# Kernel optimization log

Measured on AMD Instinct MI355X. Metric: run time of the kernel, lower is better.

Reference implementation:

```python
import jax, jax.numpy as jnp
import numpy as np

H = 1024          # hidden_size
NH = 16           # num_attention_heads
HD = H // NH      # head_dim = 64
CAUSAL_HEADS = 4  # causal_attention_heads
META_HEADS = NH // 4
B, S = 2, 2048
CVEC = 16
# static cognitive-state scalars (Python floats in the original dict)
CAUSAL_WEIGHT = 0.7   # > 0.5 -> causal branch active
AWARENESS = 0.9       # > 0.8 -> metacognitive branch active


def _mha(x, in_w, in_b, out_w, out_b, n_heads):
    """torch nn.MultiheadAttention (batch_first, self-attn, no mask, eval).
    in_w: [H, 3H] (pre-transposed), out_w: [H, H]."""
    b, s, h = x.shape
    hd = h // n_heads
    qkv = x @ in_w + in_b                      # [b, s, 3H]
    q, k, v = jnp.split(qkv, 3, axis=-1)
    def heads(t):
        return t.reshape(b, s, n_heads, hd).transpose(0, 2, 1, 3)  # [b, nh, s, hd]
    q, k, v = heads(q), heads(k), heads(v)
    scores = jnp.einsum('bhqd,bhkd->bhqk', q, k) / jnp.sqrt(jnp.float32(hd))
    probs = jax.nn.softmax(scores, axis=-1)
    ctx = jnp.einsum('bhqk,bhkd->bhqd', probs, v)
    ctx = ctx.transpose(0, 2, 1, 3).reshape(b, s, h)
    return ctx @ out_w + out_b


def setup_inputs() -> dict:
    key = jax.random.key(0)
    ks = jax.random.split(key, 20)
    w = lambda k, shp: (jax.random.normal(k, shp, dtype=jnp.float32) * 0.02)
    inp = {
        'hidden_states': jax.random.normal(ks[0], (B, S, H), dtype=jnp.float32),
        'attention_mask': jnp.ones((B, S), dtype=jnp.int32),
        'consciousness_vector': jax.random.uniform(ks[1], (CVEC,), dtype=jnp.float32),
        'Wq': w(ks[2], (H, H)), 'bq': jnp.zeros((H,), jnp.float32),
        'Wk': w(ks[3], (H, H)), 'bk': jnp.zeros((H,), jnp.float32),
        'Wv': w(ks[4], (H, H)), 'bv': jnp.zeros((H,), jnp.float32),
        'Wg': w(ks[5], (H, NH)), 'bg': jnp.zeros((NH,), jnp.float32),
        'Wa': w(ks[6], (CVEC, NH)), 'ba': jnp.zeros((NH,), jnp.float32),
        'ca_in_w': w(ks[7], (H, 3 * H)), 'ca_in_b': jnp.zeros((3 * H,), jnp.float32),
        'ca_out_w': w(ks[8], (H, H)), 'ca_out_b': jnp.zeros((H,), jnp.float32),
        'ma_in_w': w(ks[9], (H, 3 * H)), 'ma_in_b': jnp.zeros((3 * H,), jnp.float32),
        'ma_out_w': w(ks[10], (H, H)), 'ma_out_b': jnp.zeros((H,), jnp.float32),
        'Wo': w(ks[11], (H, H)), 'bo': jnp.zeros((H,), jnp.float32),
    }
    return inp


def reference(hidden_states, attention_mask, consciousness_vector,
              Wq, bq, Wk, bk, Wv, bv, Wg, bg, Wa, ba,
              ca_in_w, ca_in_b, ca_out_w, ca_out_b,
              ma_in_w, ma_in_b, ma_out_w, ma_out_b, Wo, bo):
    b, s, h = hidden_states.shape
    def heads(t):
        return t.reshape(b, s, NH, HD).transpose(0, 2, 1, 3)  # [b, NH, s, HD]
    q = heads(hidden_states @ Wq + bq)
    k = heads(hidden_states @ Wk + bk)
    v = heads(hidden_states @ Wv + bv)
    scores = jnp.einsum('bhqd,bhkd->bhqk', q, k) / jnp.sqrt(jnp.float32(HD))
    # consciousness modulation: sigmoid(gate(hs) + awareness(cvec)) -> [b, s, NH]
    gate = hidden_states @ Wg + bg
    awareness = consciousness_vector @ Wa + ba            # [NH]
    modulation = jax.nn.sigmoid(gate + awareness)         # [b, s, NH]
    # per-head, per-query-row scaling of scores ([b, NH, s, 1])
    scores = scores * modulation.transpose(0, 2, 1)[:, :, :, None]
    # mask: [b, s] -> [b, 1, 1, s]; masked positions -> -inf before softmax
    scores = jnp.where(attention_mask[:, None, None, :] == 0, -jnp.inf, scores)
    probs = jax.nn.softmax(scores, axis=-1)
    # dropout is identity in eval mode
    ctx = jnp.einsum('bhqk,bhkd->bhqd', probs, v)
    ctx = ctx.transpose(0, 2, 1, 3).reshape(b, s, h)
    # causal branch (causal_active > 0.5)
    causal_ctx = _mha(hidden_states, ca_in_w, ca_in_b, ca_out_w, ca_out_b, CAUSAL_HEADS)
    ctx = ctx * (1.0 - CAUSAL_WEIGHT) + causal_ctx * CAUSAL_WEIGHT
    # metacognitive branch (awareness_level > 0.8)
    meta_ctx = _mha(ctx, ma_in_w, ma_in_b, ma_out_w, ma_out_b, META_HEADS)
    mw = (AWARENESS - 0.8) / 0.2
    ctx = ctx * (1.0 - mw * 0.3) + meta_ctx * (mw * 0.3)
    return ctx @ Wo + bo
```

## Files before the change

kernel.cpp:

```cpp
#include <hip/hip_runtime.h>
#include <math.h>

#define HDIM 1024
#define NHEAD 16
#define SEQ   2048
#define BATCH 2
#define NROWS (BATCH * SEQ)
#define NEG_INF (-__builtin_inff())

typedef unsigned short u16;
typedef float  f32x4  __attribute__((ext_vector_type(4)));
typedef short  short8 __attribute__((ext_vector_type(8)));
typedef _Float16 half8 __attribute__((ext_vector_type(8)));

__device__ __forceinline__ u16 f2bf(float x) {
    unsigned u = __float_as_uint(x);
    unsigned r = u + 0x7fffu + ((u >> 16) & 1u);
    return (u16)(r >> 16);
}
__device__ __forceinline__ float bf2f(u16 h) { return __uint_as_float(((unsigned)h) << 16); }
__device__ __forceinline__ u16 f2h(float x) { _Float16 h = (_Float16)x; return *(u16*)&h; }

__global__ __launch_bounds__(256) void conv_f16(const float* __restrict__ src,
                                                u16* __restrict__ dst)
{
    int i8 = (blockIdx.x * 256 + threadIdx.x) * 8;
    float4 a = *(const float4*)&src[i8];
    float4 b = *(const float4*)&src[i8 + 4];
    u16 h[8] = {f2h(a.x), f2h(a.y), f2h(a.z), f2h(a.w),
                f2h(b.x), f2h(b.y), f2h(b.z), f2h(b.w)};
    uint4 p;
    p.x = h[0] | (h[1] << 16); p.y = h[2] | (h[3] << 16);
    p.z = h[4] | (h[5] << 16); p.w = h[6] | (h[7] << 16);
    *(uint4*)&dst[i8] = p;
}

__global__ __launch_bounds__(256) void convW(const float* __restrict__ Wsrc, int ldw, int n0,
                                             int dst, u16* __restrict__ WTH, u16* __restrict__ WTL)
{
    __shared__ float tile[64][65];
    int t = threadIdx.x;
    int nb = blockIdx.x * 64, kb = blockIdx.y * 64;
    #pragma unroll
    for (int i = 0; i < 4; i++) {
        int r = (t >> 4) + i * 16, cg = t & 15;
        float4 v = *(const float4*)&Wsrc[(size_t)(kb + r) * ldw + n0 + nb + cg * 4];
        tile[r][cg * 4 + 0] = v.x; tile[r][cg * 4 + 1] = v.y;
        tile[r][cg * 4 + 2] = v.z; tile[r][cg * 4 + 3] = v.w;
    }
    __syncthreads();
    int n = t & 63, g0 = (t >> 6) * 2;
    #pragma unroll
    for (int gg = 0; gg < 2; gg++) {
        int g = g0 + gg;
        u16 hi[8], lo[8];
        #pragma unroll
        for (int u = 0; u < 8; u++) {
            float x = tile[g * 8 + u][n];
            hi[u] = f2bf(x); lo[u] = f2bf(x - bf2f(hi[u]));
        }
        size_t ob = (size_t)(dst + nb + n) * 1024 + kb + g * 8;
        uint4 ph, pl;
        ph.x = hi[0] | (hi[1] << 16); ph.y = hi[2] | (hi[3] << 16);
        ph.z = hi[4] | (hi[5] << 16); ph.w = hi[6] | (hi[7] << 16);
        pl.x = lo[0] | (lo[1] << 16); pl.y = lo[2] | (lo[3] << 16);
        pl.z = lo[4] | (lo[5] << 16); pl.w = lo[6] | (lo[7] << 16);
        *(uint4*)&WTH[ob] = ph;
        *(uint4*)&WTL[ob] = pl;
    }
}

__global__ __launch_bounds__(256) void convW3_f16(
    const float* __restrict__ w0, const float* __restrict__ w1, const float* __restrict__ w2,
    int ldw, int n0s, u16* __restrict__ WT)
{
    __shared__ float tile[64][65];
    int t = threadIdx.x;
    int z = blockIdx.z;
    const float* Wsrc = (z == 0) ? w0 : (z == 1) ? w1 : w2;
    int n0 = z * n0s, dst = z * 1024;
    int nb = blockIdx.x * 64, kb = blockIdx.y * 64;
    #pragma unroll
    for (int i = 0; i < 4; i++) {
        int r = (t >> 4) + i * 16, cg = t & 15;
        float4 v = *(const float4*)&Wsrc[(size_t)(kb + r) * ldw + n0 + nb + cg * 4];
        tile[r][cg * 4 + 0] = v.x; tile[r][cg * 4 + 1] = v.y;
        tile[r][cg * 4 + 2] = v.z; tile[r][cg * 4 + 3] = v.w;
    }
    __syncthreads();
    int n = t & 63, g0 = (t >> 6) * 2;
    #pragma unroll
    for (int gg = 0; gg < 2; gg++) {
        int g = g0 + gg;
        u16 h[8];
        #pragma unroll
        for (int u = 0; u < 8; u++) h[u] = f2h(tile[g * 8 + u][n]);
        size_t ob = (size_t)(dst + nb + n) * 1024 + kb + g * 8;
        uint4 p;
        p.x = h[0] | (h[1] << 16); p.y = h[2] | (h[3] << 16);
        p.z = h[4] | (h[5] << 16); p.w = h[6] | (h[7] << 16);
        *(uint4*)&WT[ob] = p;
    }
}

__global__ __launch_bounds__(256) void transpose_f16(
    const u16* __restrict__ in, u16* __restrict__ out)
{
    __shared__ u16 th[64][72];
    int t = threadIdx.x;
    int cb = blockIdx.x * 64;
    int rb = blockIdx.y * 64;
    {
        int r = t >> 2;
        #pragma unroll
        for (int i = 0; i < 2; i++) {
            int ck = (t & 3) + 4 * i;
            *(short8*)&th[r][ck * 8] = *(const short8*)&in[(size_t)(rb + r) * 3072 + 2048 + cb + ck * 8];
        }
    }
    __syncthreads();
    int c = t & 63, g0 = (t >> 6) * 2;
    #pragma unroll
    for (int gg = 0; gg < 2; gg++) {
        int g = g0 + gg;
        u16 hv[8];
        #pragma unroll
        for (int u = 0; u < 8; u++) hv[u] = th[g * 8 + u][c];
        size_t ob = (size_t)(cb + c) * NROWS + rb + g * 8;
        uint4 ph;
        ph.x = hv[0] | (hv[1] << 16); ph.y = hv[2] | (hv[3] << 16);
        ph.z = hv[4] | (hv[5] << 16); ph.w = hv[6] | (hv[7] << 16);
        *(uint4*)&out[ob] = ph;
    }
}

__global__ __launch_bounds__(256) void gate_f32(
    const float* __restrict__ hs, const float* __restrict__ Wg,
    const float* __restrict__ bg, const float* __restrict__ cvec,
    const float* __restrict__ Wa, const float* __restrict__ ba,
    float* __restrict__ mod)
{
    __shared__ float aw[16];
    int t = threadIdx.x;
    if (t < 16) {
        float s = ba[t];
        for (int i = 0; i < 16; i++) s = fmaf(cvec[i], Wa[i * 16 + t], s);
        aw[t] = s;
    }
    __syncthreads();
    int h = t & 15;
    int r = blockIdx.x * 16 + (t >> 4);
    const float* hrow = hs + (size_t)r * HDIM;
    float s = bg[h];
    for (int k = 0; k < HDIM; k++) s = fmaf(hrow[k], Wg[k * 16 + h], s);
    s += aw[h];
    mod[(size_t)r * 16 + h] = 1.f / (1.f + __expf(-s));
}

__global__ __launch_bounds__(256, 3) void gemm_f16(
    const u16* __restrict__ A, const u16* __restrict__ BT,
    const float* __restrict__ b0, const float* __restrict__ b1, const float* __restrict__ b2,
    u16* __restrict__ out, int M, int N, int K)
{
    __shared__ u16 aS[128][40], bS[128][40];
    int t = threadIdx.x;
    int l = t & 63, w = t >> 6;
    int lane15 = l & 15, quad = l >> 4;
    int wm = (w >> 1) * 64, wn = (w & 1) * 64;
    int m0 = blockIdx.y * 128, n0 = blockIdx.x * 128;
    int sr = t >> 1;
    f32x4 acc[4][4] = {};
    short8 pa[2], pb[2];
    auto pre = [&](int k0) {
        #pragma unroll
        for (int i = 0; i < 2; i++) {
            int ck = (t & 1) * 2 + i;
            pa[i] = *(const short8*)&A[(size_t)(m0 + sr) * K + k0 + ck * 8];
            pb[i] = *(const short8*)&BT[(size_t)(n0 + sr) * K + k0 + ck * 8];
        }
    };
    pre(0);
    for (int k0 = 0; k0 < K; k0 += 32) {
        __syncthreads();
        #pragma unroll
        for (int i = 0; i < 2; i++) {
            int ck = (t & 1) * 2 + i;
            *(short8*)&aS[sr][ck * 8] = pa[i];
            *(short8*)&bS[sr][ck * 8] = pb[i];
        }
        __syncthreads();
        if (k0 + 32 < K) pre(k0 + 32);
        half8 af[4], bf[4];
        #pragma unroll
        for (int mt = 0; mt < 4; mt++)
            af[mt] = *(const half8*)&aS[wm + mt * 16 + lane15][quad * 8];
        #pragma unroll
        for (int nt = 0; nt < 4; nt++)
            bf[nt] = *(const half8*)&bS[wn + nt * 16 + lane15][quad * 8];
        #pragma unroll
        for (int mt = 0; mt < 4; mt++)
            #pragma unroll
            for (int nt = 0; nt < 4; nt++)
                acc[mt][nt] = __builtin_amdgcn_mfma_f32_16x16x32_f16(af[mt], bf[nt], acc[mt][nt], 0, 0, 0);
    }
    #pragma unroll
    for (int nt = 0; nt < 4; nt++) {
        int col = n0 + wn + nt * 16 + lane15;
        const float* bsel = (col < 1024) ? b0 : (col < 2048) ? b1 : b2;
        float bv = bsel[col & 1023];
        #pragma unroll
        for (int mt = 0; mt < 4; mt++)
            #pragma unroll
            for (int reg = 0; reg < 4; reg++) {
                int row = m0 + wm + mt * 16 + quad * 4 + reg;
                out[(size_t)row * N + col] = f2h(acc[mt][nt][reg] + bv);
            }
    }
}

__global__ __launch_bounds__(256, 2) void gemm_bf3(
    const u16* __restrict__ AH, const u16* __restrict__ AL,
    const u16* __restrict__ BTH, const u16* __restrict__ BTL,
    const float* __restrict__ bias,
    const u16* __restrict__ CinH, const u16* __restrict__ CinL,
    float* __restrict__ outF, u16* __restrict__ outH, u16* __restrict__ outL,
    u16* __restrict__ outX,
    int M, int N, int K, float alpha, float beta, int omode)
{
    __shared__ u16 aH[128][40], aL[128][40], bH[128][40], bL[128][40];
    int t = threadIdx.x;
    int l = t & 63, w = t >> 6;
    int lane15 = l & 15, quad = l >> 4;
    int wm = (w >> 1) * 64, wn = (w & 1) * 64;
    int m0 = blockIdx.y * 128, n0 = blockIdx.x * 128;
    int sr = t >> 1;
    f32x4 acc[4][4] = {};
    short8 pah[2], pal[2], pbh[2], pbl[2];

    auto pre = [&](int k0) {
        #pragma unroll
        for (int i = 0; i < 2; i++) {
            int ck = (t & 1) * 2 + i;
            size_t ga = (size_t)(m0 + sr) * K + k0 + ck * 8;
            size_t gb = (size_t)(n0 + sr) * K + k0 + ck * 8;
            pah[i] = *(const short8*)&AH[ga];
            pal[i] = *(const short8*)&AL[ga];
            pbh[i] = *(const short8*)&BTH[gb];
            pbl[i] = *(const short8*)&BTL[gb];
        }
    };
    pre(0);
    for (int k0 = 0; k0 < K; k0 += 32) {
        __syncthreads();
        #pragma unroll
        for (int i = 0; i < 2; i++) {
            int ck = (t & 1) * 2 + i;
            *(short8*)&aH[sr][ck * 8] = pah[i];
            *(short8*)&aL[sr][ck * 8] = pal[i];
            *(short8*)&bH[sr][ck * 8] = pbh[i];
            *(short8*)&bL[sr][ck * 8] = pbl[i];
        }
        __syncthreads();
        if (k0 + 32 < K) pre(k0 + 32);
        short8 afh[4], afl[4], bfh[4], bfl[4];
        #pragma unroll
        for (int mt = 0; mt < 4; mt++) {
            int r = wm + mt * 16 + lane15;
            afh[mt] = *(const short8*)&aH[r][quad * 8];
            afl[mt] = *(const short8*)&aL[r][quad * 8];
        }
        #pragma unroll
        for (int nt = 0; nt < 4; nt++) {
            int r = wn + nt * 16 + lane15;
            bfh[nt] = *(const short8*)&bH[r][quad * 8];
            bfl[nt] = *(const short8*)&bL[r][quad * 8];
        }
        #pragma unroll
        for (int mt = 0; mt < 4; mt++)
            #pragma unroll
            for (int nt = 0; nt < 4; nt++) {
                acc[mt][nt] = __builtin_amdgcn_mfma_f32_16x16x32_bf16(afh[mt], bfh[nt], acc[mt][nt], 0, 0, 0);
                acc[mt][nt] = __builtin_amdgcn_mfma_f32_16x16x32_bf16(afh[mt], bfl[nt], acc[mt][nt], 0, 0, 0);
                acc[mt][nt] = __builtin_amdgcn_mfma_f32_16x16x32_bf16(afl[mt], bfh[nt], acc[mt][nt], 0, 0, 0);
            }
    }
    #pragma unroll
    for (int nt = 0; nt < 4; nt++) {
        int col = n0 + wn + nt * 16 + lane15;
        float bv = bias[col];
        #pragma unroll
        for (int mt = 0; mt < 4; mt++) {
            #pragma unroll
            for (int reg = 0; reg < 4; reg++) {
                int row = m0 + wm + mt * 16 + quad * 4 + reg;
                size_t idx = (size_t)row * N + col;
                float v = alpha * (acc[mt][nt][reg] + bv);
                if (beta != 0.f) v += beta * (bf2f(CinH[idx]) + bf2f(CinL[idx]));
                if (omode == 0) outF[idx] = v;
                else {
                    u16 hb = f2bf(v);
                    outH[idx] = hb;
                    outL[idx] = f2bf(v - bf2f(hb));
                }
                if (outX) outX[idx] = f2h(v);
            }
        }
    }
}

__global__ __launch_bounds__(256, 3) void attn_main(
    const u16* __restrict__ QKV, const u16* __restrict__ VT,
    const float* __restrict__ modp, const int* __restrict__ maskp, float scale,
    u16* __restrict__ outH, u16* __restrict__ outL)
{
    constexpr int NT = SEQ / 128;
    constexpr int LD = 3 * HDIM;
    __shared__ __align__(16) u16 kbuf[2][128][64];
    __shared__ u16 st[4][16][132];

    int t = threadIdx.x, l = t & 63, w = t >> 6;
    int lane15 = l & 15, quad = l >> 4;
    int qt0 = blockIdx.x * 64, h = blockIdx.y, b = blockIdx.z;
    int bS_ = b * SEQ;
    int srK = t >> 1, ckK = (t & 1) * 4;
    int srV = t >> 2, ckV = (t & 3) * 4;

    half8 qf[2];
    {
        size_t qoff = (size_t)(bS_ + qt0 + w * 16 + lane15) * LD + h * 64 + quad * 8;
        qf[0] = *(const half8*)&QKV[qoff];
        qf[1] = *(const half8*)&QKV[qoff + 32];
    }
    float smod2[4];
    #pragma unroll
    for (int reg = 0; reg < 4; reg++) {
        int rw = qt0 + w * 16 + quad * 4 + reg;
        smod2[reg] = scale * 1.44269504f * modp[(size_t)(bS_ + rw) * NHEAD + h];
    }
    float lst[4] = {0.f, 0.f, 0.f, 0.f};
    f32x4 o[4] = {};

    short8 ph[4];
    auto loadK = [&](int kt) {
        size_t base = (size_t)(bS_ + kt + srK) * LD + HDIM + h * 64;
        #pragma unroll
        for (int i = 0; i < 4; i++) ph[i] = *(const short8*)&QKV[base + (ckK + i) * 8];
    };
    auto loadV = [&](int kt) {
        size_t base = (size_t)(h * 64 + srV) * NROWS + bS_ + kt;
        #pragma unroll
        for (int i = 0; i < 4; i++) ph[i] = *(const short8*)&VT[base + (ckV + i) * 8];
    };
    auto storK = [&](int pb) {
        #pragma unroll
        for (int i = 0; i < 4; i++) {
            int cw = (ckK + i) ^ (srK & 7);
            *(short8*)&kbuf[pb][srK][cw * 8] = ph[i];
        }
    };
    auto storV = [&](int pb) {
        u16* vb = &kbuf[pb][0][0];
        #pragma unroll
        for (int i = 0; i < 4; i++) {
            int cw = (ckV + i) ^ (srV & 7);
            *(short8*)&vb[srV * 128 + cw * 8] = ph[i];
        }
    };

    loadK(0); storK(0); loadV(0);
    int pb = 0;

    for (int it = 0; it < NT; it++) {
        int kt = it * 128;
        __syncthreads();
        storV(pb ^ 1);
        if (it + 1 < NT) loadK(kt + 128);
        f32x4 sacc[8] = {};
        #pragma unroll
        for (int ks = 0; ks < 2; ks++)
            #pragma unroll
            for (int nb = 0; nb < 8; nb++) {
                int r = nb * 16 + lane15;
                int cw = (ks * 4 + quad) ^ (r & 7);
                half8 kb = *(const half8*)&kbuf[pb][r][cw * 8];
                sacc[nb] = __builtin_amdgcn_mfma_f32_16x16x32_f16(qf[ks], kb, sacc[nb], 0, 0, 0);
            }
        pb ^= 1;
        #pragma unroll
        for (int nb = 0; nb < 8; nb++) {
            float kmf = maskp[bS_ + kt + nb * 16 + lane15] ? 1.f : 0.f;
            #pragma unroll
            for (int reg = 0; reg < 4; reg++) {
                float p = exp2f(fmaf(sacc[nb][reg], smod2[reg], -6.f)) * kmf;
                st[w][quad * 4 + reg][nb * 16 + lane15] = f2h(p);
                lst[reg] += p;
            }
        }
        half8 pf[4];
        #pragma unroll
        for (int ks = 0; ks < 4; ks++)
            pf[ks] = *(const half8*)&st[w][lane15][ks * 32 + quad * 8];
        __syncthreads();
        if (it + 1 < NT) { storK(pb ^ 1); loadV(kt + 128); }
        const u16* vb = &kbuf[pb][0][0];
        #pragma unroll
        for (int ks = 0; ks < 4; ks++)
            #pragma unroll
            for (int nb = 0; nb < 4; nb++) {
                int r = nb * 16 + lane15;
                int cw = (ks * 4 + quad) ^ (r & 7);
                half8 vv = *(const half8*)&vb[r * 128 + cw * 8];
                o[nb] = __builtin_amdgcn_mfma_f32_16x16x32_f16(pf[ks], vv, o[nb], 0, 0, 0);
            }
        pb ^= 1;
    }
    #pragma unroll
    for (int d = 1; d < 16; d <<= 1)
        #pragma unroll
        for (int reg = 0; reg < 4; reg++)
            lst[reg] += __shfl_xor(lst[reg], d, 64);
    #pragma unroll
    for (int reg = 0; reg < 4; reg++) {
        float inv = (lst[reg] > 0.f) ? 1.f / lst[reg] : 0.f;
        int row = qt0 + w * 16 + quad * 4 + reg;
        size_t rbase = (size_t)(bS_ + row) * HDIM + h * 64;
        #pragma unroll
        for (int nb = 0; nb < 4; nb++) {
            float v = o[nb][reg] * inv;
            size_t idx = rbase + nb * 16 + lane15;
            u16 hb = f2bf(v);
            outH[idx] = hb;
            outL[idx] = f2bf(v - bf2f(hb));
        }
    }
}

template <int NC>
__global__ __launch_bounds__(256, 2) void attn_f16(
    const u16* __restrict__ QKV, const u16* __restrict__ VT,
    float scale, u16* __restrict__ outH, u16* __restrict__ outL, int ldo)
{
    constexpr int HDT = NC * 64;
    constexpr int NT  = (SEQ / 2) / 64;
    constexpr int LD  = 3 * HDIM;
    __shared__ __align__(16) u16 kbuf[2][2][64][64];
    __shared__ u16 st[4][16][68];
    __shared__ float xl[2][16];

    int t = threadIdx.x, l = t & 63, w = t >> 6;
    int lane15 = l & 15, quad = l >> 4;
    int g = w & 1, s = w >> 1;
    int t128 = t & 127, srow = t128 >> 1, ckb = (t128 & 1) * 4;
    int qt0 = blockIdx.x * 32, h = blockIdx.y, b = blockIdx.z;
    int bS = b * SEQ, kbeg = s * (SEQ / 2);

    half8 qf[NC][2];
    {
        size_t qoff = (size_t)(bS + qt0 + g * 16 + lane15) * LD + h * HDT + quad * 8;
        #pragma unroll
        for (int c = 0; c < NC; c++)
            #pragma unroll
            for (int ks = 0; ks < 2; ks++)
                qf[c][ks] = *(const half8*)&QKV[qoff + c * 64 + ks * 32];
    }
    float sc2 = scale * 1.44269504f;
    float lst[4] = {0.f, 0.f, 0.f, 0.f};
    f32x4 o[NC][4] = {};

    short8 phv[4];
    auto loadK = [&](int c, int kt) {
        size_t base = (size_t)(bS + kt + srow) * LD + HDIM + h * HDT + c * 64;
        #pragma unroll
        for (int i = 0; i < 4; i++) phv[i] = *(const short8*)&QKV[base + (ckb + i) * 8];
    };
    auto loadV = [&](int c, int kt) {
        size_t base = (size_t)(h * HDT + c * 64 + srow) * NROWS + bS + kt;
        #pragma unroll
        for (int i = 0; i < 4; i++) phv[i] = *(const short8*)&VT[base + (ckb + i) * 8];
    };
    auto stor = [&](int pb_) {
        #pragma unroll
        for (int i = 0; i < 4; i++) {
            int ck = ckb + i, cw = ck ^ (srow & 7);
            *(short8*)&kbuf[pb_][s][srow][cw * 8] = phv[i];
        }
    };

    loadK(0, kbeg);
    stor(0);
    loadK(1, kbeg);
    int pb = 0;

    for (int it = 0; it < NT; it++) {
        int kt = kbeg + it * 64;
        f32x4 sacc[4] = {};
        #pragma unroll
        for (int c = 0; c < NC; c++) {
            __syncthreads();
            stor(pb ^ 1);
            if (c + 2 < NC) loadK(c + 2, kt);
            else if (c + 2 < 2 * NC) loadV(c + 2 - NC, kt);
            else if (it + 1 < NT) loadK(0, kt + 64);
            #pragma unroll
            for (int ks = 0; ks < 2; ks++)
                #pragma unroll
                for (int nb = 0; nb < 4; nb++) {
                    int r = nb * 16 + lane15;
                    int cw = (ks * 4 + quad) ^ (r & 7);
                    half8 kb = *(const half8*)&kbuf[pb][s][r][cw * 8];
                    sacc[nb] = __builtin_amdgcn_mfma_f32_16x16x32_f16(qf[c][ks], kb, sacc[nb], 0, 0, 0);
                }
            pb ^= 1;
        }
        #pragma unroll
        for (int nb = 0; nb < 4; nb++)
            #pragma unroll
            for (int reg = 0; reg < 4; reg++) {
                float p = exp2f(fmaf(sacc[nb][reg], sc2, -6.f));
                st[w][quad * 4 + reg][nb * 16 + lane15] = f2h(p);
                lst[reg] += p;
            }
        half8 pf[2];
        #pragma unroll
        for (int ks = 0; ks < 2; ks++)
            pf[ks] = *(const half8*)&st[w][lane15][ks * 32 + quad * 8];
        #pragma unroll
        for (int c = 0; c < NC; c++) {
            __syncthreads();
            if (it < NT - 1 || c < NC - 1) stor(pb ^ 1);
            if (c + 2 < NC) loadV(c + 2, kt);
            else if (it + 1 < NT) {
                int p2 = c + 2 - NC;
                if (p2 < NC) loadK(p2, kt + 64); else loadV(p2 - NC, kt + 64);
            }
            #pragma unroll
            for (int ks = 0; ks < 2; ks++)
                #pragma unroll
                for (int nb = 0; nb < 4; nb++) {
                    int r = nb * 16 + lane15;
                    int cw = (ks * 4 + quad) ^ (r & 7);
                    half8 vb = *(const half8*)&kbuf[pb][s][r][cw * 8];
                    o[c][nb] = __builtin_amdgcn_mfma_f32_16x16x32_f16(pf[ks], vb, o[c][nb], 0, 0, 0);
                }
            pb ^= 1;
        }
    }
    #pragma unroll
    for (int d = 1; d < 16; d <<= 1)
        #pragma unroll
        for (int reg = 0; reg < 4; reg++)
            lst[reg] += __shfl_xor(lst[reg], d, 64);
    float* xO = (float*)kbuf;
    __syncthreads();
    if (s == 1) {
        #pragma unroll
        for (int c = 0; c < NC; c++)
            #pragma unroll
            for (int nb = 0; nb < 4; nb++)
                #pragma unroll
                for (int reg = 0; reg < 4; reg++)
                    xO[(size_t)(g * 16 + quad * 4 + reg) * HDT + c * 64 + nb * 16 + lane15] = o[c][nb][reg];
        if (lane15 == 0)
            #pragma unroll
            for (int reg = 0; reg < 4; reg++)
                xl[g][quad * 4 + reg] = lst[reg];
    }
    __syncthreads();
    if (s == 0) {
        #pragma unroll
        for (int reg = 0; reg < 4; reg++) {
            float lt = lst[reg] + xl[g][quad * 4 + reg];
            float inv = (lt > 0.f) ? 1.f / lt : 0.f;
            int row = qt0 + g * 16 + quad * 4 + reg;
            size_t rbase = (size_t)(bS + row) * ldo + h * HDT;
            #pragma unroll
            for (int c = 0; c < NC; c++)
                #pragma unroll
                for (int nb = 0; nb < 4; nb++) {
                    float x1 = xO[(size_t)(g * 16 + quad * 4 + reg) * HDT + c * 64 + nb * 16 + lane15];
                    float v = (o[c][nb][reg] + x1) * inv;
                    size_t idx = rbase + c * 64 + nb * 16 + lane15;
                    u16 hb = f2bf(v);
                    outH[idx] = hb;
                    outL[idx] = f2bf(v - bf2f(hb));
                }
        }
    }
}

extern "C" void kernel_launch(void* const* d_in, const int* in_sizes, int n_in,
                              void* d_out, int out_size, void* d_ws, size_t ws_size,
                              hipStream_t stream)
{
    const float* hs   = (const float*)d_in[0];
    const int*   mask = (const int*)d_in[1];
    const float* cvec = (const float*)d_in[2];
    const float* Wq = (const float*)d_in[3];  const float* bq = (const float*)d_in[4];
    const float* Wk = (const float*)d_in[5];  const float* bk = (const float*)d_in[6];
    const float* Wv = (const float*)d_in[7];  const float* bv = (const float*)d_in[8];
    const float* Wg = (const float*)d_in[9];  const float* bg = (const float*)d_in[10];
    const float* Wa = (const float*)d_in[11]; const float* ba = (const float*)d_in[12];
    const float* caw = (const float*)d_in[13]; const float* cab = (const float*)d_in[14];
    const float* cow = (const float*)d_in[15]; const float* cob = (const float*)d_in[16];
    const float* maw = (const float*)d_in[17]; const float* mab = (const float*)d_in[18];
    const float* mow = (const float*)d_in[19]; const float* mob = (const float*)d_in[20];
    const float* Wo = (const float*)d_in[21]; const float* bo = (const float*)d_in[22];
    float* out = (float*)d_out;

    char* W = (char*)d_ws;
    const size_t MB = (size_t)1 << 20;
    u16*  QKV  = (u16*)(W + 0 * MB);
    u16*  VT   = (u16*)(W + 24 * MB);
    u16*  ctxH = (u16*)(W + 32 * MB);    u16* ctxL = (u16*)(W + 40 * MB);
    u16*  C2H  = (u16*)(W + 48 * MB);    u16* C2L  = (u16*)(W + 56 * MB);
    float* MOD = (float*)(W + 64 * MB);
    u16*  hsX  = (u16*)(W + 65 * MB);
    u16*  ctxX = (u16*)(W + 73 * MB);
    u16*  wtX  = (u16*)(W + 81 * MB);
    u16*  wtH  = (u16*)(W + 87 * MB);    u16* wtL = (u16*)(W + 89 * MB);

    dim3 blk(256);
    dim3 gw(16, 16);
    dim3 gw3(16, 16, 3);
    dim3 gt(16, 64);
    dim3 gg3(24, 32);
    dim3 gg1(8, 32);
    dim3 gaM(SEQ / 64, NHEAD, BATCH);
    dim3 gaB(SEQ / 32, 4, BATCH);

    conv_f16<<<2048, blk, 0, stream>>>(hs, hsX);
    gate_f32<<<NROWS / 16, blk, 0, stream>>>(hs, Wg, bg, cvec, Wa, ba, MOD);

    convW3_f16<<<gw3, blk, 0, stream>>>(Wq, Wk, Wv, 1024, 0, wtX);
    gemm_f16<<<gg3, blk, 0, stream>>>(hsX, wtX, bq, bk, bv, QKV, NROWS, 3072, 1024);
    transpose_f16<<<gt, blk, 0, stream>>>(QKV, VT);
    attn_main<<<gaM, blk, 0, stream>>>(QKV, VT, MOD, mask, 0.125f, ctxH, ctxL);

    convW3_f16<<<gw3, blk, 0, stream>>>(caw, caw, caw, 3072, 1024, wtX);
    gemm_f16<<<gg3, blk, 0, stream>>>(hsX, wtX, cab, cab + 1024, cab + 2048, QKV, NROWS, 3072, 1024);
    transpose_f16<<<gt, blk, 0, stream>>>(QKV, VT);
    attn_f16<4><<<gaB, blk, 0, stream>>>(QKV, VT, 0.0625f, C2H, C2L, HDIM);
    convW<<<gw, blk, 0, stream>>>(cow, 1024, 0, 0, wtH, wtL);
    gemm_bf3<<<gg1, blk, 0, stream>>>(C2H, C2L, wtH, wtL, cob,
        ctxH, ctxL, nullptr, ctxH, ctxL, ctxX, NROWS, 1024, 1024, 0.7f, 0.3f, 1);

    convW3_f16<<<gw3, blk, 0, stream>>>(maw, maw, maw, 3072, 1024, wtX);
    gemm_f16<<<gg3, blk, 0, stream>>>(ctxX, wtX, mab, mab + 1024, mab + 2048, QKV, NROWS, 3072, 1024);
    transpose_f16<<<gt, blk, 0, stream>>>(QKV, VT);
    attn_f16<4><<<gaB, blk, 0, stream>>>(QKV, VT, 0.0625f, C2H, C2L, HDIM);
    convW<<<gw, blk, 0, stream>>>(mow, 1024, 0, 0, wtH, wtL);
    gemm_bf3<<<gg1, blk, 0, stream>>>(C2H, C2L, wtH, wtL, mob,
        ctxH, ctxL, nullptr, ctxH, ctxL, nullptr, NROWS, 1024, 1024, 0.15f, 0.85f, 1);

    convW<<<gw, blk, 0, stream>>>(Wo, 1024, 0, 0, wtH, wtL);
    gemm_bf3<<<gg1, blk, 0, stream>>>(ctxH, ctxL, wtH, wtL, bo,
        nullptr, nullptr, out, nullptr, nullptr, nullptr, NROWS, 1024, 1024, 1.f, 0.f, 0);
}
```

Baseline: 709.6 us.

## Transpose QK MFMA operands so each lane owns one query row, pack P stores

Swaps the A/B operands of the score MFMA in both attention kernels, so each lane's accumulator holds four consecutive keys for a single query row. The row sum then becomes one scalar per lane, reduced with two shuffles instead of sixteen. Mask loads become one int4, and probabilities are packed to fp16 pairs and written to LDS as 8-byte stores. MFMA sections are also wrapped in s_setprio to favour matrix issue; the cost is that cvt_pkrtz rounds toward zero, which slightly changes P precision.

```diff
diff --git a/kernel.cpp b/kernel.cpp
--- a/kernel.cpp
+++ b/kernel.cpp
@@ -12,6 +12,7 @@
 typedef float  f32x4  __attribute__((ext_vector_type(4)));
 typedef short  short8 __attribute__((ext_vector_type(8)));
 typedef _Float16 half8 __attribute__((ext_vector_type(8)));
+typedef __fp16 fp16x2 __attribute__((ext_vector_type(2)));
 
 __device__ __forceinline__ u16 f2bf(float x) {
     unsigned u = __float_as_uint(x);
@@ -20,6 +21,10 @@
 }
 __device__ __forceinline__ float bf2f(u16 h) { return __uint_as_float(((unsigned)h) << 16); }
 __device__ __forceinline__ u16 f2h(float x) { _Float16 h = (_Float16)x; return *(u16*)&h; }
+__device__ __forceinline__ unsigned pkh(float a, float b) {
+    fp16x2 h = __builtin_amdgcn_cvt_pkrtz(a, b);
+    return __builtin_bit_cast(unsigned int, h);
+}
 
 __global__ __launch_bounds__(256) void conv_f16(const float* __restrict__ src,
                                                 u16* __restrict__ dst)
@@ -316,7 +321,7 @@
     constexpr int NT = SEQ / 128;
     constexpr int LD = 3 * HDIM;
     __shared__ __align__(16) u16 kbuf[2][128][64];
-    __shared__ u16 st[4][16][132];
+    __shared__ __align__(16) u16 st[4][16][132];
 
     int t = threadIdx.x, l = t & 63, w = t >> 6;
     int lane15 = l & 15, quad = l >> 4;
@@ -331,13 +336,9 @@
         qf[0] = *(const half8*)&QKV[qoff];
         qf[1] = *(const half8*)&QKV[qoff + 32];
     }
-    float smod2[4];
-    #pragma unroll
-    for (int reg = 0; reg < 4; reg++) {
-        int rw = qt0 + w * 16 + quad * 4 + reg;
-        smod2[reg] = scale * 1.44269504f * modp[(size_t)(bS_ + rw) * NHEAD + h];
-    }
-    float lst[4] = {0.f, 0.f, 0.f, 0.f};
+    float smod2 = scale * 1.44269504f *
+                  modp[(size_t)(bS_ + qt0 + w * 16 + lane15) * NHEAD + h];
+    float lst = 0.f;
     f32x4 o[4] = {};
 
     short8 ph[4];
@@ -376,6 +377,7 @@
         storV(pb ^ 1);
         if (it + 1 < NT) loadK(kt + 128);
         f32x4 sacc[8] = {};
+        __builtin_amdgcn_s_setprio(1);
         #pragma unroll
         for (int ks = 0; ks < 2; ks++)
             #pragma unroll
@@ -383,18 +385,22 @@
                 int r = nb * 16 + lane15;
                 int cw = (ks * 4 + quad) ^ (r & 7);
                 half8 kb = *(const half8*)&kbuf[pb][r][cw * 8];
-                sacc[nb] = __builtin_amdgcn_mfma_f32_16x16x32_f16(qf[ks], kb, sacc[nb], 0, 0, 0);
+                sacc[nb] = __builtin_amdgcn_mfma_f32_16x16x32_f16(kb, qf[ks], sacc[nb], 0, 0, 0);
             }
+        __builtin_amdgcn_s_setprio(0);
         pb ^= 1;
         #pragma unroll
         for (int nb = 0; nb < 8; nb++) {
-            float kmf = maskp[bS_ + kt + nb * 16 + lane15] ? 1.f : 0.f;
-            #pragma unroll
-            for (int reg = 0; reg < 4; reg++) {
-                float p = exp2f(fmaf(sacc[nb][reg], smod2[reg], -6.f)) * kmf;
-                st[w][quad * 4 + reg][nb * 16 + lane15] = f2h(p);
-                lst[reg] += p;
-            }
+            int4 mk = *(const int4*)&maskp[bS_ + kt + nb * 16 + quad * 4];
+            float p0 = exp2f(fmaf(sacc[nb][0], smod2, mk.x ? -6.f : NEG_INF));
+            float p1 = exp2f(fmaf(sacc[nb][1], smod2, mk.y ? -6.f : NEG_INF));
+            float p2 = exp2f(fmaf(sacc[nb][2], smod2, mk.z ? -6.f : NEG_INF));
+            float p3 = exp2f(fmaf(sacc[nb][3], smod2, mk.w ? -6.f : NEG_INF));
+            lst += (p0 + p1) + (p2 + p3);
+            uint2 u2;
+            u2.x = pkh(p0, p1);
+            u2.y = pkh(p2, p3);
+            *(uint2*)&st[w][lane15][nb * 16 + quad * 4] = u2;
         }
         half8 pf[4];
         #pragma unroll
@@ -403,6 +409,7 @@
         __syncthreads();
         if (it + 1 < NT) { storK(pb ^ 1); loadV(kt + 128); }
         const u16* vb = &kbuf[pb][0][0];
+        __builtin_amdgcn_s_setprio(1);
         #pragma unroll
         for (int ks = 0; ks < 4; ks++)
             #pragma unroll
@@ -412,16 +419,15 @@
                 half8 vv = *(const half8*)&vb[r * 128 + cw * 8];
                 o[nb] = __builtin_amdgcn_mfma_f32_16x16x32_f16(pf[ks], vv, o[nb], 0, 0, 0);
             }
+        __builtin_amdgcn_s_setprio(0);
         pb ^= 1;
     }
-    #pragma unroll
-    for (int d = 1; d < 16; d <<= 1)
-        #pragma unroll
-        for (int reg = 0; reg < 4; reg++)
-            lst[reg] += __shfl_xor(lst[reg], d, 64);
+    lst += __shfl_xor(lst, 16, 64);
+    lst += __shfl_xor(lst, 32, 64);
     #pragma unroll
     for (int reg = 0; reg < 4; reg++) {
-        float inv = (lst[reg] > 0.f) ? 1.f / lst[reg] : 0.f;
+        float lv = __shfl(lst, quad * 4 + reg, 64);
+        float inv = (lv > 0.f) ? 1.f / lv : 0.f;
         int row = qt0 + w * 16 + quad * 4 + reg;
         size_t rbase = (size_t)(bS_ + row) * HDIM + h * 64;
         #pragma unroll
@@ -444,7 +450,7 @@
     constexpr int NT  = (SEQ / 2) / 64;
     constexpr int LD  = 3 * HDIM;
     __shared__ __align__(16) u16 kbuf[2][2][64][64];
-    __shared__ u16 st[4][16][68];
+    __shared__ __align__(16) u16 st[4][16][68];
     __shared__ float xl[2][16];
 
     int t = threadIdx.x, l = t & 63, w = t >> 6;
@@ -464,7 +470,7 @@
                 qf[c][ks] = *(const half8*)&QKV[qoff + c * 64 + ks * 32];
     }
     float sc2 = scale * 1.44269504f;
-    float lst[4] = {0.f, 0.f, 0.f, 0.f};
+    float lst = 0.f;
     f32x4 o[NC][4] = {};
 
     short8 phv[4];
@@ -501,6 +507,7 @@
             if (c + 2 < NC) loadK(c + 2, kt);
             else if (c + 2 < 2 * NC) loadV(c + 2 - NC, kt);
             else if (it + 1 < NT) loadK(0, kt + 64);
+            __builtin_amdgcn_s_setprio(1);
             #pragma unroll
             for (int ks = 0; ks < 2; ks++)
                 #pragma unroll
@@ -508,18 +515,23 @@
                     int r = nb * 16 + lane15;
                     int cw = (ks * 4 + quad) ^ (r & 7);
                     half8 kb = *(const half8*)&kbuf[pb][s][r][cw * 8];
-                    sacc[nb] = __builtin_amdgcn_mfma_f32_16x16x32_f16(qf[c][ks], kb, sacc[nb], 0, 0, 0);
+                    sacc[nb] = __builtin_amdgcn_mfma_f32_16x16x32_f16(kb, qf[c][ks], sacc[nb], 0, 0, 0);
                 }
+            __builtin_amdgcn_s_setprio(0);
             pb ^= 1;
         }
         #pragma unroll
-        for (int nb = 0; nb < 4; nb++)
-            #pragma unroll
-            for (int reg = 0; reg < 4; reg++) {
-                float p = exp2f(fmaf(sacc[nb][reg], sc2, -6.f));
-                st[w][quad * 4 + reg][nb * 16 + lane15] = f2h(p);
-                lst[reg] += p;
-            }
+        for (int nb = 0; nb < 4; nb++) {
+            float p0 = exp2f(fmaf(sacc[nb][0], sc2, -6.f));
+            float p1 = exp2f(fmaf(sacc[nb][1], sc2, -6.f));
+            float p2 = exp2f(fmaf(sacc[nb][2], sc2, -6.f));
+            float p3 = exp2f(fmaf(sacc[nb][3], sc2, -6.f));
+            lst += (p0 + p1) + (p2 + p3);
+            uint2 u2;
+            u2.x = pkh(p0, p1);
+            u2.y = pkh(p2, p3);
+            *(uint2*)&st[w][lane15][nb * 16 + quad * 4] = u2;
+        }
         half8 pf[2];
         #pragma unroll
         for (int ks = 0; ks < 2; ks++)
@@ -533,6 +545,7 @@
                 int p2 = c + 2 - NC;
                 if (p2 < NC) loadK(p2, kt + 64); else loadV(p2 - NC, kt + 64);
             }
+            __builtin_amdgcn_s_setprio(1);
             #pragma unroll
             for (int ks = 0; ks < 2; ks++)
                 #pragma unroll
@@ -542,14 +555,12 @@
                     half8 vb = *(const half8*)&kbuf[pb][s][r][cw * 8];
                     o[c][nb] = __builtin_amdgcn_mfma_f32_16x16x32_f16(pf[ks], vb, o[c][nb], 0, 0, 0);
                 }
+            __builtin_amdgcn_s_setprio(0);
             pb ^= 1;
         }
     }
-    #pragma unroll
-    for (int d = 1; d < 16; d <<= 1)
-        #pragma unroll
-        for (int reg = 0; reg < 4; reg++)
-            lst[reg] += __shfl_xor(lst[reg], d, 64);
+    lst += __shfl_xor(lst, 16, 64);
+    lst += __shfl_xor(lst, 32, 64);
     float* xO = (float*)kbuf;
     __syncthreads();
     if (s == 1) {
@@ -560,16 +571,13 @@
                 #pragma unroll
                 for (int reg = 0; reg < 4; reg++)
                     xO[(size_t)(g * 16 + quad * 4 + reg) * HDT + c * 64 + nb * 16 + lane15] = o[c][nb][reg];
-        if (lane15 == 0)
-            #pragma unroll
-            for (int reg = 0; reg < 4; reg++)
-                xl[g][quad * 4 + reg] = lst[reg];
+        if (quad == 0) xl[g][lane15] = lst;
     }
     __syncthreads();
     if (s == 0) {
         #pragma unroll
         for (int reg = 0; reg < 4; reg++) {
-            float lt = lst[reg] + xl[g][quad * 4 + reg];
+            float lt = __shfl(lst, quad * 4 + reg, 64) + xl[g][quad * 4 + reg];
             float inv = (lt > 0.f) ? 1.f / lt : 0.f;
             int row = qt0 + g * 16 + quad * 4 + reg;
             size_t rbase = (size_t)(bS + row) * ldo + h * HDT;
```

New measurement: 720.7 us. About the same (+1.6%).
